# Kernel optimization log

Hardware: AMD Instinct MI355X
Metric: run time of the kernel (lower is better)

## Reference

```python
import jax, jax.numpy as jnp
import numpy as np

N_NODES = 20000
N_EDGES = 320000
B, F_IN, H_DIM, P = 4, 16, 64, 12


def _glorot(key, shape):
    fan_in, fan_out = shape[0], shape[-1]
    lim = float(np.sqrt(6.0 / (fan_in + fan_out)))
    return jax.random.uniform(key, shape, jnp.float32, -lim, lim)


def setup_inputs() -> dict:
    key = jax.random.key(0)
    ks = jax.random.split(key, 20)
    x = jax.random.normal(ks[0], (B, N_NODES, F_IN, P), jnp.float32)
    edge_index = jax.random.randint(ks[1], (2, N_EDGES), 0, N_NODES, jnp.int64)
    edge_weight = jax.random.uniform(ks[2], (N_EDGES,), jnp.float32)
    # GCNConv weights (in, out) and biases for z/r/h gates
    Wg_z = _glorot(ks[3], (F_IN, H_DIM)); bg_z = jnp.zeros((H_DIM,), jnp.float32)
    Wg_r = _glorot(ks[4], (F_IN, H_DIM)); bg_r = jnp.zeros((H_DIM,), jnp.float32)
    Wg_h = _glorot(ks[5], (F_IN, H_DIM)); bg_h = jnp.zeros((H_DIM,), jnp.float32)
    # Linear layers on concat([conv_out, H]) -> (2H, H)
    Wl_z = _glorot(ks[6], (2 * H_DIM, H_DIM)); bl_z = jax.random.uniform(ks[7], (H_DIM,), jnp.float32, -0.1, 0.1)
    Wl_r = _glorot(ks[8], (2 * H_DIM, H_DIM)); bl_r = jax.random.uniform(ks[9], (H_DIM,), jnp.float32, -0.1, 0.1)
    Wl_h = _glorot(ks[10], (2 * H_DIM, H_DIM)); bl_h = jax.random.uniform(ks[11], (H_DIM,), jnp.float32, -0.1, 0.1)
    att = jax.random.uniform(ks[12], (P,), jnp.float32)  # attention logits over periods
    W_out = _glorot(ks[13], (H_DIM, P)); b_out = jax.random.uniform(ks[14], (P,), jnp.float32, -0.1, 0.1)
    return {"x": x, "edge_index": edge_index, "edge_weight": edge_weight,
            "Wg_z": Wg_z, "bg_z": bg_z, "Wg_r": Wg_r, "bg_r": bg_r, "Wg_h": Wg_h, "bg_h": bg_h,
            "Wl_z": Wl_z, "bl_z": bl_z, "Wl_r": Wl_r, "bl_r": bl_r, "Wl_h": Wl_h, "bl_h": bl_h,
            "att": att, "W_out": W_out, "b_out": b_out}


def reference(x, edge_index, edge_weight, Wg_z, bg_z, Wg_r, bg_r, Wg_h, bg_h,
              Wl_z, bl_z, Wl_r, bl_r, Wl_h, bl_h, att, W_out, b_out):
    Bsz, N, F, Pn = x.shape
    Hh = Wg_z.shape[1]
    # --- gcn_norm: add self loops (weight 1.0), D^-1/2 (A+I) D^-1/2 ---
    loop = jnp.arange(N)
    src = jnp.concatenate([edge_index[0], loop])
    dst = jnp.concatenate([edge_index[1], loop])
    w = jnp.concatenate([edge_weight, jnp.ones((N,), x.dtype)])
    deg = jnp.zeros((N,), x.dtype).at[dst].add(w)
    dinv = jnp.where(deg > 0, jax.lax.rsqrt(deg), 0.0)
    norm = dinv[src] * w * dinv[dst]  # (E+N,)
    # --- propagate raw features once for all periods: (A_hat X) W == A_hat (X W) ---
    xf = x.reshape(Bsz, N, F * Pn)
    msg = xf[:, src, :] * norm[None, :, None]            # (B, E+N, F*P) gather
    agg = jnp.zeros((Bsz, N, F * Pn), x.dtype).at[:, dst, :].add(msg)  # scatter-add
    agg = agg.reshape(Bsz, N, F, Pn)
    # --- A3TGCN2: per-period single GRU step from H=0, attention-pooled ---
    probs = jax.nn.softmax(att)
    H0 = jnp.zeros((Bsz, N, Hh), x.dtype)

    def step(acc, inp):
        a, p = inp  # a: (B, N, F) aggregated features of this period
        cz = a @ Wg_z + bg_z
        cr = a @ Wg_r + bg_r
        ch = a @ Wg_h + bg_h
        Z = jax.nn.sigmoid(jnp.concatenate([cz, H0], -1) @ Wl_z + bl_z)
        R = jax.nn.sigmoid(jnp.concatenate([cr, H0], -1) @ Wl_r + bl_r)
        Ht = jnp.tanh(jnp.concatenate([ch, H0 * R], -1) @ Wl_h + bl_h)
        Hn = Z * H0 + (1.0 - Z) * Ht
        return acc + p * Hn, None

    a_seq = jnp.moveaxis(agg, -1, 0)  # (P, B, N, F)
    Hacc, _ = jax.lax.scan(step, H0, (a_seq, probs))
    # --- trailing ReLU + Linear ---
    return jax.nn.relu(Hacc) @ W_out + b_out  # (B, N, P)
```

## Files before the change

### kernel.cpp

```cpp
#include <hip/hip_runtime.h>
#include <cstdint>
#include <cstddef>

#define NN 20000
#define NE 320000
#define NB 4
#define NF 16
#define NH 64
#define NP 12
#define FP (NF*NP)
#define ROWB (FP*2)
#define NROWB (NB*ROWB)
#define GRID_MAIN 2000

typedef _Float16 h2_t __attribute__((ext_vector_type(2)));
typedef _Float16 h4_t __attribute__((ext_vector_type(4)));
typedef float    f4_t __attribute__((ext_vector_type(4)));

union U32H2 { unsigned u; h2_t h; };
union U64H4 { uint2 u; h4_t h; };

__global__ __launch_bounds__(256) void k_pre1(const float* __restrict__ x,
                                              _Float16* __restrict__ xh,
                                              const int* __restrict__ ei,
                                              const float* __restrict__ ew,
                                              float* deg, int* counts) {
    int blk = blockIdx.x;
    if (blk < 15000) {
        int i = blk * 256 + threadIdx.x;
        int b = i / (NN * 48);
        int rem = i - b * (NN * 48);
        int n = rem / 48;
        int c = rem - n * 48;
        float4 v = ((const float4*)x)[i];
        h4_t o = { (_Float16)v.x, (_Float16)v.y, (_Float16)v.z, (_Float16)v.w };
        ((h4_t*)xh)[(n * NB + b) * 48 + c] = o;
    } else {
        int e = (blk - 15000) * 256 + threadIdx.x;
        int dst = ei[NE + e];
        atomicAdd(&deg[dst], ew[e]);
        atomicAdd(&counts[dst], 1);
    }
}

__global__ __launch_bounds__(1024) void k_prep(
        const float* __restrict__ deg, float* __restrict__ dinv,
        const int* __restrict__ counts, int* __restrict__ offsets,
        const float* __restrict__ Wg_z, const float* __restrict__ bg_z,
        const float* __restrict__ Wg_h, const float* __restrict__ bg_h,
        const float* __restrict__ Wl_z, const float* __restrict__ bl_z,
        const float* __restrict__ Wl_h, const float* __restrict__ bl_h,
        const float* __restrict__ att, const float* __restrict__ W_out,
        uint2* __restrict__ wfrag, uint2* __restrict__ wofrag,
        float* bz_eff, float* bh_eff, float* probs) {
    __shared__ float wzl[NF][NH + 1];
    __shared__ float whl[NF][NH + 1];
    int blk = blockIdx.x;
    int t = threadIdx.x;
    if (blk < 20) {
        int i = blk * 1024 + t;
        if (i < NN) dinv[i] = rsqrtf(1.0f + deg[i]);
        return;
    }
    if (blk == 20) {
        __shared__ int sums[1024];
        const int PER = (NN + 1023) / 1024;
        int start = t * PER;
        int end   = start + PER; if (end > NN) end = NN;
        int s = 0;
        for (int i = start; i < end && start < NN; ++i) s += counts[i];
        if (start >= NN) s = 0;
        sums[t] = s;
        __syncthreads();
        for (int off = 1; off < 1024; off <<= 1) {
            int v = (t >= off) ? sums[t - off] : 0;
            __syncthreads();
            sums[t] += v;
            __syncthreads();
        }
        int run = (t == 0) ? 0 : sums[t - 1];
        for (int i = start; i < end && start < NN; ++i) { offsets[i] = run + i; run += counts[i]; }
        if (t == 1023) offsets[NN] = sums[1023] + NN;
        return;
    }
    {
        int f = t >> 6, j = t & 63;
        float sz = 0.f, sh = 0.f;
        for (int k = 0; k < NH; ++k) {
            sz += Wg_z[f * NH + k] * Wl_z[k * NH + j];
            sh += Wg_h[f * NH + k] * Wl_h[k * NH + j];
        }
        wzl[f][j] = sz;
        whl[f][j] = sh;
    }
    if (t < NH) {
        float bz = bl_z[t], bh = bl_h[t];
        for (int k = 0; k < NH; ++k) {
            bz += bg_z[k] * Wl_z[k * NH + t];
            bh += bg_h[k] * Wl_h[k * NH + t];
        }
        bz_eff[t] = bz;
        bh_eff[t] = bh;
    }
    if (t == 0) {
        float m = att[0];
        for (int p = 1; p < NP; ++p) m = fmaxf(m, att[p]);
        float s = 0.f, e_[NP];
        for (int p = 0; p < NP; ++p) { e_[p] = expf(att[p] - m); s += e_[p]; }
        for (int p = 0; p < 16; ++p) probs[p] = (p < NP) ? e_[p] / s : 0.f;
    }
    __syncthreads();
    if (t < 512) {
        int ln = t & 63, c = (t >> 6) & 3, zh = t >> 8;
        int kb = 4 * (ln >> 4);
        int j  = 16 * c + (ln & 15);
        float v0, v1, v2, v3;
        if (zh == 0) { v0 = wzl[kb][j]; v1 = wzl[kb+1][j]; v2 = wzl[kb+2][j]; v3 = wzl[kb+3][j]; }
        else         { v0 = whl[kb][j]; v1 = whl[kb+1][j]; v2 = whl[kb+2][j]; v3 = whl[kb+3][j]; }
        union { _Float16 h[4]; uint2 u; } pk;
        pk.h[0] = (_Float16)v0; pk.h[1] = (_Float16)v1;
        pk.h[2] = (_Float16)v2; pk.h[3] = (_Float16)v3;
        wfrag[(zh * 4 + c) * 64 + ln] = pk.u;
    }
    if (t < 256) {
        int ln = t & 63, s = t >> 6;
        int kj = 16 * s + 4 * (ln >> 4);
        int nn_ = ln & 15;
        union { _Float16 h[4]; uint2 u; } pk;
        for (int i = 0; i < 4; ++i)
            pk.h[i] = (_Float16)((nn_ < NP) ? W_out[(kj + i) * NP + nn_] : 0.f);
        wofrag[s * 64 + ln] = pk.u;
    }
}

__global__ __launch_bounds__(256) void k_fill(const int* __restrict__ ei,
                                              const float* __restrict__ ew,
                                              const float* __restrict__ dinv,
                                              const int* __restrict__ offsets,
                                              int* cursor, uint2* __restrict__ erec) {
    int e = blockIdx.x * 256 + threadIdx.x;
    if (e < NE) {
        int s = ei[e];
        int d = ei[NE + e];
        float nm = dinv[s] * ew[e] * dinv[d];
        int pos = atomicAdd(&cursor[d], 1);
        int idx = offsets[d] + pos;
        _Float16 hn = (_Float16)nm;
        U32H2 w; w.h = (h2_t){hn, hn};
        erec[idx] = make_uint2((unsigned)(s * NROWB), w.u);
    } else if (e < NE + NN) {
        int node = e - NE;
        float di = dinv[node];
        _Float16 hn = (_Float16)(di * di);
        U32H2 w; w.h = (h2_t){hn, hn};
        erec[offsets[node + 1] - 1] = make_uint2((unsigned)(node * NROWB), w.u);
    }
}

__global__ __launch_bounds__(256) void k_main(
        const _Float16* __restrict__ xh,
        const int* __restrict__ offsets, const uint2* __restrict__ erec,
        const uint2* __restrict__ wfrag, const uint2* __restrict__ wofrag,
        const float* __restrict__ bz_eff, const float* __restrict__ bh_eff,
        const float* __restrict__ probs, const float* __restrict__ b_out,
        float* __restrict__ out) {
    __shared__ _Float16 a_lds[NB][FP];
    __shared__ _Float16 r_lds[2][NB][NH + 8];
    __shared__ uint2    wz_lds[512];
    __shared__ uint2    wo_lds[256];
    __shared__ float    bzh_lds[128];
    __shared__ float    pr_lds[16];
    __shared__ float    bo_lds[12];

    int t = threadIdx.x;
    wz_lds[t]       = wfrag[t];
    wz_lds[t + 256] = wfrag[t + 256];
    wo_lds[t]       = wofrag[t];
    if (t < 128) bzh_lds[t] = (t < 64) ? bz_eff[t] : bh_eff[t - 64];
    if (t < 16)  pr_lds[t] = probs[t];
    if (t < 12)  bo_lds[t] = b_out[t];
    __syncthreads();

    int b = t >> 6;
    int lane = t & 63;
    int half = lane >> 5;
    int g = lane >> 4, p = lane & 15;

    const char* xbase = (const char*)xh;
    int lb = b * ROWB + (lane & 31) * 12;

    int it = 0;
    for (int n = blockIdx.x; n < NN; n += GRID_MAIN, ++it) {
        int beg = offsets[n], end = offsets[n + 1];
        int last = end - 1;

        h2_t A0 = {(_Float16)0.f, (_Float16)0.f};
        h2_t A1 = A0, A2 = A0;

        uint2 qa0, qa1, qa2, qa3, qa4, qa5, qa6, qa7;
        {
            int e0 = beg;
#define LQ(K, QV) { int s_ = e0 + 2*(K) + half; int i_ = s_ < last ? s_ : last; QV = erec[i_]; }
            LQ(0,qa0) LQ(1,qa1) LQ(2,qa2) LQ(3,qa3) LQ(4,qa4) LQ(5,qa5) LQ(6,qa6) LQ(7,qa7)
#undef LQ
        }

        int ecur = beg;
        while (true) {
            int enext = ecur + 16;
            bool more = enext < end;
            uint2 qb0, qb1, qb2, qb3, qb4, qb5, qb6, qb7;
            if (more) {
#define LQ(K, QV) { int s_ = enext + 2*(K) + half; int i_ = s_ < last ? s_ : last; QV = erec[i_]; }
                LQ(0,qb0) LQ(1,qb1) LQ(2,qb2) LQ(3,qb3) LQ(4,qb4) LQ(5,qb5) LQ(6,qb6) LQ(7,qb7)
#undef LQ
            }
            uint3 u0 = *(const uint3*)(xbase + qa0.x + lb);
            uint3 u1 = *(const uint3*)(xbase + qa1.x + lb);
            uint3 u2 = *(const uint3*)(xbase + qa2.x + lb);
            uint3 u3 = *(const uint3*)(xbase + qa3.x + lb);
            uint3 u4 = *(const uint3*)(xbase + qa4.x + lb);
            uint3 u5 = *(const uint3*)(xbase + qa5.x + lb);
            uint3 u6 = *(const uint3*)(xbase + qa6.x + lb);
            uint3 u7 = *(const uint3*)(xbase + qa7.x + lb);
#define ACC(K, QV, UV) { \
                int s_ = ecur + 2*(K) + half; \
                unsigned w_ = (s_ <= last) ? QV.y : 0u; \
                U32H2 wu; wu.u = w_; \
                U32H2 x0; x0.u = UV.x; U32H2 x1; x1.u = UV.y; U32H2 x2; x2.u = UV.z; \
                A0 += wu.h * x0.h; A1 += wu.h * x1.h; A2 += wu.h * x2.h; }
            ACC(0,qa0,u0) ACC(1,qa1,u1) ACC(2,qa2,u2) ACC(3,qa3,u3)
            ACC(4,qa4,u4) ACC(5,qa5,u5) ACC(6,qa6,u6) ACC(7,qa7,u7)
#undef ACC
            if (!more) break;
            qa0=qb0; qa1=qb1; qa2=qb2; qa3=qb3; qa4=qb4; qa5=qb5; qa6=qb6; qa7=qb7;
            ecur = enext;
        }

        {
            U32H2 t0, t1, t2, s0, s1, s2;
            t0.h = A0; t1.h = A1; t2.h = A2;
            s0.u = (unsigned)__shfl_xor((int)t0.u, 32, 64);
            s1.u = (unsigned)__shfl_xor((int)t1.u, 32, 64);
            s2.u = (unsigned)__shfl_xor((int)t2.u, 32, 64);
            A0 += s0.h; A1 += s1.h; A2 += s2.h;
        }

        if (lane < 32) {
            unsigned* aw = (unsigned*)&a_lds[b][0];
            U32H2 t0, t1, t2; t0.h = A0; t1.h = A1; t2.h = A2;
            int L = lane;
            aw[3 * L + 0] = t0.u;
            aw[3 * L + 1] = t1.u;
            aw[3 * L + 2] = t2.u;
        }

        int pe = (p < NP) ? p : 0;
        const _Float16* ab = &a_lds[b][48 * g + pe];
        h4_t A = { ab[0], ab[12], ab[24], ab[36] };

        f4_t accz[4], acch[4];
#pragma unroll
        for (int c = 0; c < 4; ++c) {
            float bzv = bzh_lds[16 * c + p];
            float bhv = bzh_lds[64 + 16 * c + p];
            accz[c] = (f4_t){bzv, bzv, bzv, bzv};
            acch[c] = (f4_t){bhv, bhv, bhv, bhv};
        }
#pragma unroll
        for (int c = 0; c < 4; ++c) {
            U64H4 fz; fz.u = wz_lds[c * 64 + lane];
            U64H4 fh; fh.u = wz_lds[(4 + c) * 64 + lane];
            accz[c] = __builtin_amdgcn_mfma_f32_16x16x16f16(A, fz.h, accz[c], 0, 0, 0);
            acch[c] = __builtin_amdgcn_mfma_f32_16x16x16f16(A, fh.h, acch[c], 0, 0, 0);
        }

#pragma unroll
        for (int c = 0; c < 4; ++c) {
            float partial = 0.f;
#pragma unroll
            for (int r = 0; r < 4; ++r) {
                float zz = accz[c][r];
                float hh = acch[c][r];
                float sn = __builtin_amdgcn_rcpf(1.f + __expf(zz));
                float th = 1.f - 2.f * __builtin_amdgcn_rcpf(__expf(2.f * hh) + 1.f);
                partial = fmaf(pr_lds[4 * g + r], sn * th, partial);
            }
            partial += __shfl_xor(partial, 16, 64);
            partial += __shfl_xor(partial, 32, 64);
            if (g == 0) r_lds[it & 1][b][16 * c + p] = (_Float16)fmaxf(partial, 0.f);
        }
        __syncthreads();

        if (t < 64) {
            float bo = bo_lds[p < NP ? p : 0];
            f4_t co = (f4_t){bo, bo, bo, bo};
            int pb = p & 3;
#pragma unroll
            for (int s = 0; s < 4; ++s) {
                h4_t Ao = *(const h4_t*)&r_lds[it & 1][pb][16 * s + 4 * g];
                U64H4 Bo; Bo.u = wo_lds[s * 64 + lane];
                co = __builtin_amdgcn_mfma_f32_16x16x16f16(Ao, Bo.h, co, 0, 0, 0);
            }
            if (g == 0 && p < NP) {
                size_t baseo = (size_t)n * NP + p;
#pragma unroll
                for (int r = 0; r < 4; ++r)
                    out[(size_t)r * ((size_t)NN * NP) + baseo] = co[r];
            }
        }
    }
}


extern "C" void kernel_launch(void* const* d_in, const int* in_sizes, int n_in,
                              void* d_out, int out_size, void* d_ws, size_t ws_size,
                              hipStream_t stream) {
    const float* x     = (const float*)d_in[0];
    const int*   ei    = (const int*)d_in[1];
    const float* ew    = (const float*)d_in[2];
    const float* Wg_z  = (const float*)d_in[3];
    const float* bg_z  = (const float*)d_in[4];
    const float* Wg_h  = (const float*)d_in[7];
    const float* bg_h  = (const float*)d_in[8];
    const float* Wl_z  = (const float*)d_in[9];
    const float* bl_z  = (const float*)d_in[10];
    const float* Wl_h  = (const float*)d_in[13];
    const float* bl_h  = (const float*)d_in[14];
    const float* att   = (const float*)d_in[15];
    const float* W_out = (const float*)d_in[16];
    const float* b_out = (const float*)d_in[17];
    float*       out   = (float*)d_out;

    char* p = (char*)d_ws;
    auto alloc = [&](size_t bytes) -> void* {
        void* r = (void*)p;
        p += (bytes + 255) & ~(size_t)255;
        return r;
    };
    const size_t PAD_NN = ((size_t)NN * 4 + 255) & ~(size_t)255;
    float*     deg     = (float*)alloc(NN * 4);
    int*       counts  = (int*)  alloc(NN * 4);
    int*       cursor  = (int*)  alloc(NN * 4);
    float*     dinv    = (float*)alloc(NN * 4);
    int*       offsets = (int*)  alloc((NN + 1) * 4);
    uint2*     erec    = (uint2*)alloc((size_t)(NE + NN) * 8);
    uint2*     wfrag   = (uint2*)alloc(512 * 8);
    uint2*     wofrag  = (uint2*)alloc(256 * 8);
    float*     bz_eff  = (float*)alloc(NH * 4);
    float*     bh_eff  = (float*)alloc(NH * 4);
    float*     probs   = (float*)alloc(16 * 4);
    _Float16*  xh      = (_Float16*)alloc((size_t)NN * NROWB);

    hipMemsetAsync(deg, 0, PAD_NN * 3, stream);

    k_pre1 <<<16250, 256, 0, stream>>>(x, xh, ei, ew, deg, counts);
    k_prep <<<22, 1024, 0, stream>>>(deg, dinv, counts, offsets,
                                     Wg_z, bg_z, Wg_h, bg_h, Wl_z, bl_z, Wl_h, bl_h,
                                     att, W_out, wfrag, wofrag, bz_eff, bh_eff, probs);
    k_fill <<<(NE + NN + 255) / 256, 256, 0, stream>>>(ei, ew, dinv, offsets, cursor, erec);
    k_main <<<GRID_MAIN, 256, 0, stream>>>(xh, offsets, erec,
                                           wfrag, wofrag, bz_eff, bh_eff, probs, b_out, out);
}
```

Baseline: 189.0 us.

## Pad per-node edge lists to multiples of 32 and unroll gather without bounds checks

Rounds each node's CSR segment up to a multiple of 32 with zeroed records, placing the self loop after the real edges. The main aggregation loop then loads 32 edge records per iteration with full unrolling and no clamping or masking, replacing the double-buffered prefetch loop. This removes per-edge bounds logic but adds a large memset of the padded edge buffer and extra dummy loads for low-degree nodes, and it loses the overlap of record prefetch with gathers.

```diff
diff --git a/kernel.cpp b/kernel.cpp
--- a/kernel.cpp
+++ b/kernel.cpp
@@ -1,4 +1,5 @@
 #include <hip/hip_runtime.h>
+#include <hip/hip_fp16.h>
 #include <cstdint>
 #include <cstddef>
 
@@ -12,12 +13,12 @@
 #define ROWB (FP*2)
 #define NROWB (NB*ROWB)
 #define GRID_MAIN 2000
-
-typedef _Float16 h2_t __attribute__((ext_vector_type(2)));
+#define EREC_MAX (NE + 32 * NN)
+
 typedef _Float16 h4_t __attribute__((ext_vector_type(4)));
 typedef float    f4_t __attribute__((ext_vector_type(4)));
 
-union U32H2 { unsigned u; h2_t h; };
+union U32H2 { unsigned u; __half2 h; };
 union U64H4 { uint2 u; h4_t h; };
 
 __global__ __launch_bounds__(256) void k_pre1(const float* __restrict__ x,
@@ -68,7 +69,7 @@
         int start = t * PER;
         int end   = start + PER; if (end > NN) end = NN;
         int s = 0;
-        for (int i = start; i < end && start < NN; ++i) s += counts[i];
+        for (int i = start; i < end && start < NN; ++i) s += (counts[i] + 32) & ~31;
         if (start >= NN) s = 0;
         sums[t] = s;
         __syncthreads();
@@ -79,8 +80,11 @@
             __syncthreads();
         }
         int run = (t == 0) ? 0 : sums[t - 1];
-        for (int i = start; i < end && start < NN; ++i) { offsets[i] = run + i; run += counts[i]; }
-        if (t == 1023) offsets[NN] = sums[1023] + NN;
+        for (int i = start; i < end && start < NN; ++i) {
+            offsets[i] = run;
+            run += (counts[i] + 32) & ~31;
+        }
+        if (t == 1023) offsets[NN] = sums[1023];
         return;
     }
     {
@@ -137,6 +141,7 @@
                                               const float* __restrict__ ew,
                                               const float* __restrict__ dinv,
                                               const int* __restrict__ offsets,
+                                              const int* __restrict__ counts,
                                               int* cursor, uint2* __restrict__ erec) {
     int e = blockIdx.x * 256 + threadIdx.x;
     if (e < NE) {
@@ -145,15 +150,15 @@
         float nm = dinv[s] * ew[e] * dinv[d];
         int pos = atomicAdd(&cursor[d], 1);
         int idx = offsets[d] + pos;
-        _Float16 hn = (_Float16)nm;
-        U32H2 w; w.h = (h2_t){hn, hn};
+        __half hn = __float2half(nm);
+        U32H2 w; w.h = __half2(hn, hn);
         erec[idx] = make_uint2((unsigned)(s * NROWB), w.u);
     } else if (e < NE + NN) {
         int node = e - NE;
         float di = dinv[node];
-        _Float16 hn = (_Float16)(di * di);
-        U32H2 w; w.h = (h2_t){hn, hn};
-        erec[offsets[node + 1] - 1] = make_uint2((unsigned)(node * NROWB), w.u);
+        __half hn = __float2half(di * di);
+        U32H2 w; w.h = __half2(hn, hn);
+        erec[offsets[node] + counts[node]] = make_uint2((unsigned)(node * NROWB), w.u);
     }
 }
 
@@ -192,49 +197,27 @@
     int it = 0;
     for (int n = blockIdx.x; n < NN; n += GRID_MAIN, ++it) {
         int beg = offsets[n], end = offsets[n + 1];
-        int last = end - 1;
-
-        h2_t A0 = {(_Float16)0.f, (_Float16)0.f};
-        h2_t A1 = A0, A2 = A0;
-
-        uint2 qa0, qa1, qa2, qa3, qa4, qa5, qa6, qa7;
-        {
-            int e0 = beg;
-#define LQ(K, QV) { int s_ = e0 + 2*(K) + half; int i_ = s_ < last ? s_ : last; QV = erec[i_]; }
-            LQ(0,qa0) LQ(1,qa1) LQ(2,qa2) LQ(3,qa3) LQ(4,qa4) LQ(5,qa5) LQ(6,qa6) LQ(7,qa7)
-#undef LQ
-        }
-
-        int ecur = beg;
-        while (true) {
-            int enext = ecur + 16;
-            bool more = enext < end;
-            uint2 qb0, qb1, qb2, qb3, qb4, qb5, qb6, qb7;
-            if (more) {
-#define LQ(K, QV) { int s_ = enext + 2*(K) + half; int i_ = s_ < last ? s_ : last; QV = erec[i_]; }
-                LQ(0,qb0) LQ(1,qb1) LQ(2,qb2) LQ(3,qb3) LQ(4,qb4) LQ(5,qb5) LQ(6,qb6) LQ(7,qb7)
-#undef LQ
+
+        __half2 A0 = __half2(__half(0.f), __half(0.f));
+        __half2 A1 = A0, A2 = A0;
+
+        for (int e = beg; e < end; e += 32) {
+            uint2 q[16];
+#pragma unroll
+            for (int k = 0; k < 16; ++k) q[k] = erec[e + 2 * k + half];
+            uint3 u[16];
+#pragma unroll
+            for (int k = 0; k < 16; ++k) u[k] = *(const uint3*)(xbase + q[k].x + lb);
+#pragma unroll
+            for (int k = 0; k < 16; ++k) {
+                U32H2 w;  w.u  = q[k].y;
+                U32H2 x0; x0.u = u[k].x;
+                U32H2 x1; x1.u = u[k].y;
+                U32H2 x2; x2.u = u[k].z;
+                A0 = __hfma2(w.h, x0.h, A0);
+                A1 = __hfma2(w.h, x1.h, A1);
+                A2 = __hfma2(w.h, x2.h, A2);
             }
-            uint3 u0 = *(const uint3*)(xbase + qa0.x + lb);
-            uint3 u1 = *(const uint3*)(xbase + qa1.x + lb);
-            uint3 u2 = *(const uint3*)(xbase + qa2.x + lb);
-            uint3 u3 = *(const uint3*)(xbase + qa3.x + lb);
-            uint3 u4 = *(const uint3*)(xbase + qa4.x + lb);
-            uint3 u5 = *(const uint3*)(xbase + qa5.x + lb);
-            uint3 u6 = *(const uint3*)(xbase + qa6.x + lb);
-            uint3 u7 = *(const uint3*)(xbase + qa7.x + lb);
-#define ACC(K, QV, UV) { \
-                int s_ = ecur + 2*(K) + half; \
-                unsigned w_ = (s_ <= last) ? QV.y : 0u; \
-                U32H2 wu; wu.u = w_; \
-                U32H2 x0; x0.u = UV.x; U32H2 x1; x1.u = UV.y; U32H2 x2; x2.u = UV.z; \
-                A0 += wu.h * x0.h; A1 += wu.h * x1.h; A2 += wu.h * x2.h; }
-            ACC(0,qa0,u0) ACC(1,qa1,u1) ACC(2,qa2,u2) ACC(3,qa3,u3)
-            ACC(4,qa4,u4) ACC(5,qa5,u5) ACC(6,qa6,u6) ACC(7,qa7,u7)
-#undef ACC
-            if (!more) break;
-            qa0=qb0; qa1=qb1; qa2=qb2; qa3=qb3; qa4=qb4; qa5=qb5; qa6=qb6; qa7=qb7;
-            ecur = enext;
         }
 
         {
@@ -243,7 +226,7 @@
             s0.u = (unsigned)__shfl_xor((int)t0.u, 32, 64);
             s1.u = (unsigned)__shfl_xor((int)t1.u, 32, 64);
             s2.u = (unsigned)__shfl_xor((int)t2.u, 32, 64);
-            A0 += s0.h; A1 += s1.h; A2 += s2.h;
+            A0 = __hadd2(A0, s0.h); A1 = __hadd2(A1, s1.h); A2 = __hadd2(A2, s2.h);
         }
 
         if (lane < 32) {
@@ -344,7 +327,7 @@
     int*       cursor  = (int*)  alloc(NN * 4);
     float*     dinv    = (float*)alloc(NN * 4);
     int*       offsets = (int*)  alloc((NN + 1) * 4);
-    uint2*     erec    = (uint2*)alloc((size_t)(NE + NN) * 8);
+    uint2*     erec    = (uint2*)alloc((size_t)EREC_MAX * 8);
     uint2*     wfrag   = (uint2*)alloc(512 * 8);
     uint2*     wofrag  = (uint2*)alloc(256 * 8);
     float*     bz_eff  = (float*)alloc(NH * 4);
@@ -353,12 +336,13 @@
     _Float16*  xh      = (_Float16*)alloc((size_t)NN * NROWB);
 
     hipMemsetAsync(deg, 0, PAD_NN * 3, stream);
+    hipMemsetAsync(erec, 0, (size_t)EREC_MAX * 8, stream);
 
     k_pre1 <<<16250, 256, 0, stream>>>(x, xh, ei, ew, deg, counts);
     k_prep <<<22, 1024, 0, stream>>>(deg, dinv, counts, offsets,
                                      Wg_z, bg_z, Wg_h, bg_h, Wl_z, bl_z, Wl_h, bl_h,
                                      att, W_out, wfrag, wofrag, bz_eff, bh_eff, probs);
-    k_fill <<<(NE + NN + 255) / 256, 256, 0, stream>>>(ei, ew, dinv, offsets, cursor, erec);
+    k_fill <<<(NE + NN + 255) / 256, 256, 0, stream>>>(ei, ew, dinv, offsets, counts, cursor, erec);
     k_main <<<GRID_MAIN, 256, 0, stream>>>(xh, offsets, erec,
                                            wfrag, wofrag, bz_eff, bh_eff, probs, b_out, out);
 }
```

New measurement: 218.4 us. +15.5%, slower.

## Split fused gather+GRU kernel into separate gather and GRU kernels

Applied to the files above, without the earlier changes.

Splits the single fused kernel into a wave-per-(node,batch) gather kernel that writes aggregated fp16 features to a global buffer, and a separate GRU/MFMA kernel that reads them back. The aim is to decouple the irregular, latency-bound gather from the compute stage so each gets its own grid and occupancy, and no LDS or block barriers are needed in the gather. The cost is an extra global round-trip of about 30 MB, one extra kernel launch, and uncoalesced strided element loads in the GRU kernel.

```diff
diff --git a/kernel.cpp b/kernel.cpp
--- a/kernel.cpp
+++ b/kernel.cpp
@@ -11,6 +11,7 @@
 #define FP (NF*NP)
 #define ROWB (FP*2)
 #define NROWB (NB*ROWB)
+#define GRIDA 5000
 #define GRID_MAIN 2000
 
 typedef _Float16 h2_t __attribute__((ext_vector_type(2)));
@@ -157,40 +158,20 @@
     }
 }
 
-__global__ __launch_bounds__(256) void k_main(
+__global__ __launch_bounds__(256) void k_gather(
         const _Float16* __restrict__ xh,
         const int* __restrict__ offsets, const uint2* __restrict__ erec,
-        const uint2* __restrict__ wfrag, const uint2* __restrict__ wofrag,
-        const float* __restrict__ bz_eff, const float* __restrict__ bh_eff,
-        const float* __restrict__ probs, const float* __restrict__ b_out,
-        float* __restrict__ out) {
-    __shared__ _Float16 a_lds[NB][FP];
-    __shared__ _Float16 r_lds[2][NB][NH + 8];
-    __shared__ uint2    wz_lds[512];
-    __shared__ uint2    wo_lds[256];
-    __shared__ float    bzh_lds[128];
-    __shared__ float    pr_lds[16];
-    __shared__ float    bo_lds[12];
-
-    int t = threadIdx.x;
-    wz_lds[t]       = wfrag[t];
-    wz_lds[t + 256] = wfrag[t + 256];
-    wo_lds[t]       = wofrag[t];
-    if (t < 128) bzh_lds[t] = (t < 64) ? bz_eff[t] : bh_eff[t - 64];
-    if (t < 16)  pr_lds[t] = probs[t];
-    if (t < 12)  bo_lds[t] = b_out[t];
-    __syncthreads();
-
-    int b = t >> 6;
-    int lane = t & 63;
+        _Float16* __restrict__ aout) {
+    int lane = threadIdx.x & 63;
     int half = lane >> 5;
-    int g = lane >> 4, p = lane & 15;
-
+    int L = lane & 31;
+    int lb0 = L * 12;
+    int wav = (blockIdx.x << 2) + (threadIdx.x >> 6);
     const char* xbase = (const char*)xh;
-    int lb = b * ROWB + (lane & 31) * 12;
-
-    int it = 0;
-    for (int n = blockIdx.x; n < NN; n += GRID_MAIN, ++it) {
+
+    for (int u = wav; u < NN * NB; u += GRIDA * 4) {
+        int n = u >> 2, b = u & 3;
+        int lb = b * ROWB + lb0;
         int beg = offsets[n], end = offsets[n + 1];
         int last = end - 1;
 
@@ -237,27 +218,52 @@
             ecur = enext;
         }
 
-        {
-            U32H2 t0, t1, t2, s0, s1, s2;
-            t0.h = A0; t1.h = A1; t2.h = A2;
-            s0.u = (unsigned)__shfl_xor((int)t0.u, 32, 64);
-            s1.u = (unsigned)__shfl_xor((int)t1.u, 32, 64);
-            s2.u = (unsigned)__shfl_xor((int)t2.u, 32, 64);
-            A0 += s0.h; A1 += s1.h; A2 += s2.h;
-        }
+        U32H2 t0, t1, t2, s0, s1, s2;
+        t0.h = A0; t1.h = A1; t2.h = A2;
+        s0.u = (unsigned)__shfl_xor((int)t0.u, 32, 64);
+        s1.u = (unsigned)__shfl_xor((int)t1.u, 32, 64);
+        s2.u = (unsigned)__shfl_xor((int)t2.u, 32, 64);
+        t0.h += s0.h; t1.h += s1.h; t2.h += s2.h;
 
         if (lane < 32) {
-            unsigned* aw = (unsigned*)&a_lds[b][0];
-            U32H2 t0, t1, t2; t0.h = A0; t1.h = A1; t2.h = A2;
-            int L = lane;
-            aw[3 * L + 0] = t0.u;
-            aw[3 * L + 1] = t1.u;
-            aw[3 * L + 2] = t2.u;
-        }
-
+            uint3 w3; w3.x = t0.u; w3.y = t1.u; w3.z = t2.u;
+            *(uint3*)((char*)aout + (size_t)u * ROWB + lb0) = w3;
+        }
+    }
+}
+
+__global__ __launch_bounds__(256) void k_gru(
+        const _Float16* __restrict__ aout,
+        const uint2* __restrict__ wfrag, const uint2* __restrict__ wofrag,
+        const float* __restrict__ bz_eff, const float* __restrict__ bh_eff,
+        const float* __restrict__ probs, const float* __restrict__ b_out,
+        float* __restrict__ out) {
+    __shared__ _Float16 r_lds[2][NB][NH + 8];
+    __shared__ uint2    wz_lds[512];
+    __shared__ uint2    wo_lds[256];
+    __shared__ float    bzh_lds[128];
+    __shared__ float    pr_lds[16];
+    __shared__ float    bo_lds[12];
+
+    int t = threadIdx.x;
+    wz_lds[t]       = wfrag[t];
+    wz_lds[t + 256] = wfrag[t + 256];
+    wo_lds[t]       = wofrag[t];
+    if (t < 128) bzh_lds[t] = (t < 64) ? bz_eff[t] : bh_eff[t - 64];
+    if (t < 16)  pr_lds[t] = probs[t];
+    if (t < 12)  bo_lds[t] = b_out[t];
+    __syncthreads();
+
+    int b = t >> 6;
+    int lane = t & 63;
+    int g = lane >> 4, p = lane & 15;
+
+    int it = 0;
+    for (int n = blockIdx.x; n < NN; n += GRID_MAIN, ++it) {
         int pe = (p < NP) ? p : 0;
-        const _Float16* ab = &a_lds[b][48 * g + pe];
-        h4_t A = { ab[0], ab[12], ab[24], ab[36] };
+        const _Float16* arow = aout + ((size_t)n * NB + b) * FP;
+        h4_t A = { arow[(4*g + 0) * 12 + pe], arow[(4*g + 1) * 12 + pe],
+                   arow[(4*g + 2) * 12 + pe], arow[(4*g + 3) * 12 + pe] };
 
         f4_t accz[4], acch[4];
 #pragma unroll
@@ -351,14 +357,16 @@
     float*     bh_eff  = (float*)alloc(NH * 4);
     float*     probs   = (float*)alloc(16 * 4);
     _Float16*  xh      = (_Float16*)alloc((size_t)NN * NROWB);
+    _Float16*  aout    = (_Float16*)alloc((size_t)NN * NROWB);
 
     hipMemsetAsync(deg, 0, PAD_NN * 3, stream);
 
-    k_pre1 <<<16250, 256, 0, stream>>>(x, xh, ei, ew, deg, counts);
-    k_prep <<<22, 1024, 0, stream>>>(deg, dinv, counts, offsets,
-                                     Wg_z, bg_z, Wg_h, bg_h, Wl_z, bl_z, Wl_h, bl_h,
-                                     att, W_out, wfrag, wofrag, bz_eff, bh_eff, probs);
-    k_fill <<<(NE + NN + 255) / 256, 256, 0, stream>>>(ei, ew, dinv, offsets, cursor, erec);
-    k_main <<<GRID_MAIN, 256, 0, stream>>>(xh, offsets, erec,
-                                           wfrag, wofrag, bz_eff, bh_eff, probs, b_out, out);
-}
+    k_pre1   <<<16250, 256, 0, stream>>>(x, xh, ei, ew, deg, counts);
+    k_prep   <<<22, 1024, 0, stream>>>(deg, dinv, counts, offsets,
+                                       Wg_z, bg_z, Wg_h, bg_h, Wl_z, bl_z, Wl_h, bl_h,
+                                       att, W_out, wfrag, wofrag, bz_eff, bh_eff, probs);
+    k_fill   <<<(NE + NN + 255) / 256, 256, 0, stream>>>(ei, ew, dinv, offsets, cursor, erec);
+    k_gather <<<GRIDA, 256, 0, stream>>>(xh, offsets, erec, aout);
+    k_gru    <<<GRID_MAIN, 256, 0, stream>>>(aout, wfrag, wofrag,
+                                             bz_eff, bh_eff, probs, b_out, out);
+}
```

Result: slower. 221.9 us (+17.4%).
